# Kernel tuning notes

Hardware: AMD Instinct MI355X
Metric: run time of the kernel (lower is better)

The kernel has to match this reference:

```python
import jax, jax.numpy as jnp
import numpy as np
import math

B, S, D, H = 2, 2048, 1024, 16
DK = D // H


def setup_inputs() -> dict:
    key = jax.random.key(0)
    ks = jax.random.split(key, 11)
    f = jnp.float32
    return {
        "query": jax.random.normal(ks[0], (B, S, D), f),
        "key": jax.random.normal(ks[1], (B, S, D), f),
        "value": jax.random.normal(ks[2], (B, S, D), f),
        "wq": jax.random.normal(ks[3], (D, D), f) * 0.02,
        "bq": jnp.zeros((D,), f),
        "wk": jax.random.normal(ks[4], (D, D), f) * 0.02,
        "bk": jnp.zeros((D,), f),
        "wv": jax.random.normal(ks[5], (D, D), f) * 0.02,
        "bv": jnp.zeros((D,), f),
        "wo": jax.random.normal(ks[6], (D, D), f) * 0.02,
        "bo": jnp.zeros((D,), f),
    }


def reference(query, key, value, wq, bq, wk, bk, wv, bv, wo, bo):
    # Linear projections (torch Linear: y = x @ W.T + b)
    q = query @ wq.T + bq
    k = key @ wk.T + bk
    v = value @ wv.T + bv
    # [B,S,D] -> [B,H,S,DK]
    q = q.reshape(B, S, H, DK).transpose(0, 2, 1, 3)
    k = k.reshape(B, S, H, DK).transpose(0, 2, 1, 3)
    v = v.reshape(B, S, H, DK).transpose(0, 2, 1, 3)
    scores = jnp.einsum("bhqd,bhkd->bhqk", q, k) / math.sqrt(DK)
    causal = jnp.triu(jnp.ones((S, S), dtype=bool), k=1)  # strict upper triangle masked
    scores = jnp.where(causal, -jnp.inf, scores)
    attn = jax.nn.softmax(scores, axis=-1)  # dropout is identity in eval (p=0)
    x = jnp.einsum("bhqk,bhkd->bhqd", attn, v)
    x = x.transpose(0, 2, 1, 3).reshape(B, S, D)
    return x @ wo.T + bo
```

## Files before the change

kernel.cpp:

```cpp
#include <hip/hip_runtime.h>
#include <math.h>

#define BB 2
#define SS 2048
#define DD 1024
#define HH 16
#define DKK 64
#define MM (BB * SS)
#define KK DD
#define VSTR 2176

typedef __attribute__((ext_vector_type(8))) short short8;
typedef __attribute__((ext_vector_type(4))) float floatx4;

__device__ inline unsigned short f2bf(float x) {
    unsigned int u = __float_as_uint(x);
    u += 0x7fffu + ((u >> 16) & 1u);
    return (unsigned short)(u >> 16);
}

__device__ inline unsigned int pkbf(float a, float b) {
    return (__float_as_uint(b) & 0xffff0000u) | (__float_as_uint(a) >> 16);
}

__device__ inline unsigned int pkbf_rne(float a, float b) {
    return (unsigned int)f2bf(a) | ((unsigned int)f2bf(b) << 16);
}

__device__ inline unsigned int cvtpk(float a, float b) {
    unsigned int r;
    asm("v_cvt_pk_bf16_f32 %0, %1, %2" : "=v"(r) : "v"(a), "v"(b));
    return r;
}

__device__ inline void cast4f(const float* __restrict__ in, unsigned short* __restrict__ out, int i) {
    const float4 v = *(const float4*)(in + i);
    unsigned long long pk = (unsigned long long)f2bf(v.x)
                          | ((unsigned long long)f2bf(v.y) << 16)
                          | ((unsigned long long)f2bf(v.z) << 32)
                          | ((unsigned long long)f2bf(v.w) << 48);
    *(unsigned long long*)(out + i) = pk;
}

__global__ __launch_bounds__(256) void cast_all(const float* __restrict__ q, const float* __restrict__ k,
                                                const float* __restrict__ v,
                                                const float* __restrict__ wq, const float* __restrict__ wk,
                                                const float* __restrict__ wv, const float* __restrict__ wo,
                                                unsigned short* __restrict__ oq, unsigned short* __restrict__ ok,
                                                unsigned short* __restrict__ ov,
                                                unsigned short* __restrict__ owq, unsigned short* __restrict__ owk,
                                                unsigned short* __restrict__ owv, unsigned short* __restrict__ owo) {
    const int blk = blockIdx.x;
    const float* in;
    unsigned short* out;
    int idx;
    if (blk < 12288) {
        const int w = blk >> 12;
        idx = blk & 4095;
        in  = (w == 0) ? q : (w == 1) ? k : v;
        out = (w == 0) ? oq : (w == 1) ? ok : ov;
    } else {
        const int w = (blk - 12288) >> 10;
        idx = (blk - 12288) & 1023;
        in  = (w == 0) ? wq : (w == 1) ? wk : (w == 2) ? wv : wo;
        out = (w == 0) ? owq : (w == 1) ? owk : (w == 2) ? owv : owo;
    }
    cast4f(in, out, (idx * 256 + threadIdx.x) * 4);
}

#define GLDS(gp, lp) __builtin_amdgcn_global_load_lds( \
    (const __attribute__((address_space(1))) void*)(gp), \
    (__attribute__((address_space(3))) void*)(lp), 16, 0, 0)

#define SCHED0() __builtin_amdgcn_sched_barrier(0)
#define BAR()    __builtin_amdgcn_s_barrier()
#define WAITL0() asm volatile("s_waitcnt lgkmcnt(0)" ::: "memory")
#define WAITV(n) asm volatile("s_waitcnt vmcnt(" #n ")" ::: "memory")

template<int BN, int SWAP>
__device__ __forceinline__ void gemm_body2(const unsigned short* __restrict__ A,
                                           const unsigned short* __restrict__ W,
                                           int m0, int n0,
                                           unsigned short* __restrict__ As,
                                           unsigned short* __restrict__ Bs,
                                           floatx4 (&acc)[4][BN / 32]) {
    constexpr int NJ = BN / 32;
    const int t    = threadIdx.x;
    const int lane = t & 63;
    const int wave = t >> 6;
    const int col  = lane & 15;
    const int quad = lane >> 4;
    const int wm   = (wave >> 1) * 64;
    const int wn   = (wave & 1) * (BN / 2);

    const int r  = t >> 3;
    const int cs = t & 7;

    const int sA0 = (quad ^ (col & 7)) * 8;
    const int sA1 = ((quad + 4) ^ (col & 7)) * 8;

    auto stage = [&](int kt, int pb) {
        const int k0 = kt * 64;
        #pragma unroll
        for (int g = 0; g < 4; ++g) {
            const int row = g * 32 + r;
            const int ksw = (cs ^ (row & 7)) * 8;
            GLDS(A + (size_t)(m0 + row) * KK + k0 + ksw,
                 &As[pb * (128 * 64) + row * 64 + cs * 8]);
        }
        #pragma unroll
        for (int g = 0; g < BN / 32; ++g) {
            const int row = g * 32 + r;
            const int ksw = (cs ^ (row & 7)) * 8;
            GLDS(W + (size_t)(n0 + row) * KK + k0 + ksw,
                 &Bs[pb * (BN * 64) + row * 64 + cs * 8]);
        }
    };

    const int NK = KK / 64;

    auto tile_step = [&](int kt, int p) {
        if (kt + 1 < NK) stage(kt + 1, p ^ 1);

        const unsigned short* Ab = &As[p * (128 * 64)];
        const unsigned short* Bb = &Bs[p * (BN * 64)];
        short8 a0[4], a1[4], b0[NJ], b1[NJ];
        #pragma unroll
        for (int i = 0; i < 4; ++i) {
            const unsigned short* ar = Ab + (wm + i * 16 + col) * 64;
            a0[i] = *(const short8*)(ar + sA0);
            a1[i] = *(const short8*)(ar + sA1);
        }
        #pragma unroll
        for (int j = 0; j < NJ; ++j) {
            const unsigned short* br = Bb + (wn + j * 16 + col) * 64;
            b0[j] = *(const short8*)(br + sA0);
            b1[j] = *(const short8*)(br + sA1);
        }

        __builtin_amdgcn_s_setprio(1);
        #pragma unroll
        for (int i = 0; i < 4; ++i)
            #pragma unroll
            for (int j = 0; j < NJ; ++j) {
                if constexpr (SWAP)
                    acc[i][j] = __builtin_amdgcn_mfma_f32_16x16x32_bf16(b0[j], a0[i], acc[i][j], 0, 0, 0);
                else
                    acc[i][j] = __builtin_amdgcn_mfma_f32_16x16x32_bf16(a0[i], b0[j], acc[i][j], 0, 0, 0);
            }
        #pragma unroll
        for (int i = 0; i < 4; ++i)
            #pragma unroll
            for (int j = 0; j < NJ; ++j) {
                if constexpr (SWAP)
                    acc[i][j] = __builtin_amdgcn_mfma_f32_16x16x32_bf16(b1[j], a1[i], acc[i][j], 0, 0, 0);
                else
                    acc[i][j] = __builtin_amdgcn_mfma_f32_16x16x32_bf16(a1[i], b1[j], acc[i][j], 0, 0, 0);
            }
        __builtin_amdgcn_s_setprio(0);

        WAITL0(); SCHED0();
        if (kt + 1 < NK) { WAITV(0); }
        SCHED0(); BAR(); SCHED0();
    };

    stage(0, 0);
    WAITV(0); SCHED0(); BAR(); SCHED0();

    #pragma unroll 1
    for (int kt = 0; kt < NK; kt += 2) {
        tile_step(kt, 0);
        tile_step(kt + 1, 1);
    }
}

__global__ __launch_bounds__(256, 2) void gemm_qkv(const unsigned short* __restrict__ qB,
                                                   const unsigned short* __restrict__ kB,
                                                   const unsigned short* __restrict__ vB,
                                                   const unsigned short* __restrict__ wqB,
                                                   const unsigned short* __restrict__ wkB,
                                                   const unsigned short* __restrict__ wvB,
                                                   const float* __restrict__ bq,
                                                   const float* __restrict__ bk,
                                                   const float* __restrict__ bv,
                                                   unsigned short* __restrict__ Qh,
                                                   unsigned short* __restrict__ Kh,
                                                   unsigned short* __restrict__ Vt) {
    __shared__ __align__(16) unsigned short As[2 * 128 * 64];
    __shared__ __align__(16) unsigned short Bs[2 * 128 * 64];

    const int bid   = blockIdx.x;
    const int wgid  = (bid & 7) * 96 + (bid >> 3);
    const int which = wgid >> 8;
    const int tile  = wgid & 255;
    const int m0    = (tile >> 3) * 128;
    const int n0    = (tile & 7) * 128;

    const unsigned short* A = (which == 0) ? qB : (which == 1) ? kB : vB;
    const unsigned short* W = (which == 0) ? wqB : (which == 1) ? wkB : wvB;
    const float* bias       = (which == 0) ? bq : (which == 1) ? bk : bv;

    const int t    = threadIdx.x;
    const int lane = t & 63;
    const int wave = t >> 6;
    const int col  = lane & 15;
    const int quad = lane >> 4;
    const int wm   = (wave >> 1) * 64;
    const int wn   = (wave & 1) * 64;

    floatx4 acc[4][4] = {};

    if (which != 2) {
        gemm_body2<128, 1>(A, W, m0, n0, As, Bs, acc);
        unsigned short* O = (which == 0) ? Qh : Kh;
        #pragma unroll
        for (int i = 0; i < 4; ++i) {
            const int mb  = m0 + wm + i * 16 + col;
            const int bdx = mb >> 11, s = mb & 2047;
            #pragma unroll
            for (int j = 0; j < 4; ++j) {
                const int n  = n0 + wn + j * 16 + quad * 4;
                const float4 b4 = *(const float4*)(bias + n);
                const int h = n >> 6, dk = n & 63;
                uint2 w;
                w.x = pkbf_rne(acc[i][j][0] + b4.x, acc[i][j][1] + b4.y);
                w.y = pkbf_rne(acc[i][j][2] + b4.z, acc[i][j][3] + b4.w);
                *(uint2*)(O + (((size_t)(bdx * HH + h)) * SS + s) * DKK + dk) = w;
            }
        }
    } else {
        gemm_body2<128, 0>(A, W, m0, n0, As, Bs, acc);
        #pragma unroll
        for (int i = 0; i < 4; ++i) {
            #pragma unroll
            for (int j = 0; j < 4; ++j) {
                const int n  = n0 + wn + j * 16 + col;
                const float bv0 = bias[n];
                const int h = n >> 6, dk = n & 63;
                const int mb  = m0 + wm + i * 16 + quad * 4;
                const int bdx = mb >> 11, s = mb & 2047;
                unsigned short* vp = Vt + (((size_t)(bdx * HH + h)) * DKK + dk) * VSTR + s;
                uint2 w;
                w.x = pkbf_rne(acc[i][j][0] + bv0, acc[i][j][1] + bv0);
                w.y = pkbf_rne(acc[i][j][2] + bv0, acc[i][j][3] + bv0);
                *(uint2*)vp = w;
            }
        }
    }
}

__global__ __launch_bounds__(256, 2) void gemm_out(const unsigned short* __restrict__ A,
                                                   const unsigned short* __restrict__ W,
                                                   const float* __restrict__ bias,
                                                   float* __restrict__ C) {
    __shared__ __align__(16) unsigned short As[2 * 128 * 64];
    __shared__ __align__(16) unsigned short Bs[2 * 64 * 64];

    const int bid  = blockIdx.x;
    const int wgid = (bid & 7) * 64 + (bid >> 3);
    const int m0   = (wgid >> 4) * 128;
    const int n0   = (wgid & 15) * 64;

    floatx4 acc[4][2] = {};
    gemm_body2<64, 0>(A, W, m0, n0, As, Bs, acc);

    const int t    = threadIdx.x;
    const int lane = t & 63;
    const int wave = t >> 6;
    const int col  = lane & 15;
    const int quad = lane >> 4;
    const int wm   = (wave >> 1) * 64;
    const int wn   = (wave & 1) * 32;

    #pragma unroll
    for (int i = 0; i < 4; ++i) {
        #pragma unroll
        for (int j = 0; j < 2; ++j) {
            const int n = n0 + wn + j * 16 + col;
            const float bv0 = bias[n];
            #pragma unroll
            for (int rr = 0; rr < 4; ++rr) {
                const int m = m0 + wm + i * 16 + quad * 4 + rr;
                C[(size_t)m * DD + n] = acc[i][j][rr] + bv0;
            }
        }
    }
}

#define C1 0.18033688011112042f
#define C2 11.541560327111707f
#define MFMA __builtin_amdgcn_mfma_f32_16x16x32_bf16

__global__ __launch_bounds__(512, 4) void attn_mfma(const unsigned short* __restrict__ Qh,
                                                    const unsigned short* __restrict__ Kh,
                                                    const unsigned short* __restrict__ Vt,
                                                    unsigned short* __restrict__ X) {
    __shared__ __align__(16) unsigned short Ks[2][64 * 64];
    __shared__ __align__(16) unsigned short Vs[2][64 * 64];
    __shared__ __align__(16) unsigned short Plds[8][16 * 40];

    const int t    = threadIdx.x;
    const int lane = t & 63;
    const int wave = t >> 6;
    const int col  = lane & 15;
    const int quad = lane >> 4;

    const int lin = blockIdx.x;
    const int bh  = (lin & 7) + 8 * ((lin >> 3) & 3);
    const int pr  = lin >> 5;
    const int b   = bh / HH, h = bh % HH;

    const int cX  = (wave < 4) ? (31 - pr) : pr;
    const int q0  = cX * 64 + (wave & 3) * 16;
    const int nst = 32 - pr;

    const unsigned short* Kb = Kh + (size_t)bh * SS * DKK;
    const unsigned short* Vb = Vt + (size_t)bh * DKK * VSTR;

    const int r0  = t >> 3;
    const int sg0 = ((t & 7) ^ (r0 & 7)) * 8;

    unsigned short* Pw = &Plds[wave][0];

    const unsigned short* Qb = Qh + ((size_t)bh * SS + q0) * DKK;
    const short8 qa0 = *(const short8*)(Qb + (size_t)col * DKK + quad * 8);
    const short8 qa1 = *(const short8*)(Qb + (size_t)col * DKK + 32 + quad * 8);

    floatx4 o0 = {0.f, 0.f, 0.f, 0.f}, o1 = o0, o2 = o0, o3 = o0;
    floatx4 olp = {0.f, 0.f, 0.f, 0.f};

    const short8 vone = { (short)0x3F80, (short)0x3F80, (short)0x3F80, (short)0x3F80,
                          (short)0x3F80, (short)0x3F80, (short)0x3F80, (short)0x3F80 };

    const int ksA = ((quad)      ^ (col & 7)) * 8;
    const int ksB = ((quad | 4)  ^ (col & 7)) * 8;

    auto half_body = [&](const unsigned short* Kp, const unsigned short* Vp, int kb) {
        #pragma unroll
        for (int hh = 0; hh < 2; ++hh) {
            const int j0 = kb * 64 + hh * 32;
            if (j0 < q0 + 16) {
                const short8 k0 = *(const short8*)(Kp + (hh * 32 + col) * 64 + ksA);
                const short8 k1 = *(const short8*)(Kp + (hh * 32 + col) * 64 + ksB);
                const short8 k2 = *(const short8*)(Kp + (hh * 32 + col + 16) * 64 + ksA);
                const short8 k3 = *(const short8*)(Kp + (hh * 32 + col + 16) * 64 + ksB);

                floatx4 t0 = {0.f, 0.f, 0.f, 0.f}, t1 = t0;
                __builtin_amdgcn_s_setprio(1);
                t0 = MFMA(k0, qa0, t0, 0, 0, 0);
                t0 = MFMA(k1, qa1, t0, 0, 0, 0);
                t1 = MFMA(k2, qa0, t1, 0, 0, 0);
                t1 = MFMA(k3, qa1, t1, 0, 0, 0);
                __builtin_amdgcn_s_setprio(0);

                float p[8];
                if (j0 + 31 > q0) {
                    const int lim = q0 + col - j0;
                    #pragma unroll
                    for (int rr = 0; rr < 4; ++rr) {
                        p[rr]     = (quad * 4 + rr      <= lim) ? __builtin_exp2f(fmaf(t0[rr], C1, -C2)) : 0.f;
                        p[4 + rr] = (16 + quad * 4 + rr <= lim) ? __builtin_exp2f(fmaf(t1[rr], C1, -C2)) : 0.f;
                    }
                } else {
                    #pragma unroll
                    for (int rr = 0; rr < 4; ++rr) {
                        p[rr]     = __builtin_exp2f(fmaf(t0[rr], C1, -C2));
                        p[4 + rr] = __builtin_exp2f(fmaf(t1[rr], C1, -C2));
                    }
                }

                uint2 w0 = { cvtpk(p[0], p[1]), cvtpk(p[2], p[3]) };
                uint2 w1 = { cvtpk(p[4], p[5]), cvtpk(p[6], p[7]) };
                *(uint2*)(Pw + col * 40 + quad * 4)      = w0;
                *(uint2*)(Pw + col * 40 + 16 + quad * 4) = w1;

                const short8 pb = *(const short8*)(Pw + col * 40 + quad * 8);
                const int vs = hh ? ksB : ksA;
                const short8 v0 = *(const short8*)(Vp + (col)      * 64 + vs);
                const short8 v1 = *(const short8*)(Vp + (col + 16) * 64 + vs);
                const short8 v2 = *(const short8*)(Vp + (col + 32) * 64 + vs);
                const short8 v3 = *(const short8*)(Vp + (col + 48) * 64 + vs);
                __builtin_amdgcn_s_setprio(1);
                o0  = MFMA(v0, pb, o0, 0, 0, 0);
                o1  = MFMA(v1, pb, o1, 0, 0, 0);
                o2  = MFMA(v2, pb, o2, 0, 0, 0);
                o3  = MFMA(v3, pb, o3, 0, 0, 0);
                olp = MFMA(vone, pb, olp, 0, 0, 0);
                __builtin_amdgcn_s_setprio(0);
            }
        }
    };

    auto step = [&](int kb, int cur) {
        __syncthreads();
        if (kb + 1 < nst) {
            const int jn = (kb + 1) * 64;
            const int nx = cur ^ 1;
            GLDS(Kb + (size_t)(jn + r0) * DKK + sg0,  &Ks[nx][t * 8]);
            GLDS(Vb + (size_t)r0 * VSTR + jn + sg0,   &Vs[nx][t * 8]);
        }
        half_body(&Ks[cur][0], &Vs[cur][0], kb);
    };

    GLDS(Kb + (size_t)r0 * DKK + sg0,  &Ks[0][t * 8]);
    GLDS(Vb + (size_t)r0 * VSTR + sg0, &Vs[0][t * 8]);

    #pragma unroll 1
    for (int kb = 0; kb < nst; kb += 2) {
        step(kb, 0);
        if (kb + 1 < nst) step(kb + 1, 1);
    }

    const float li = 1.f / olp[0];

    unsigned short* Xp = X + ((size_t)(b * SS + q0 + col)) * DD + h * DKK + quad * 4;
    {
        uint2 w;
        w.x = cvtpk(o0[0] * li, o0[1] * li);
        w.y = cvtpk(o0[2] * li, o0[3] * li);
        *(uint2*)(Xp + 0) = w;
        w.x = cvtpk(o1[0] * li, o1[1] * li);
        w.y = cvtpk(o1[2] * li, o1[3] * li);
        *(uint2*)(Xp + 16) = w;
        w.x = cvtpk(o2[0] * li, o2[1] * li);
        w.y = cvtpk(o2[2] * li, o2[3] * li);
        *(uint2*)(Xp + 32) = w;
        w.x = cvtpk(o3[0] * li, o3[1] * li);
        w.y = cvtpk(o3[2] * li, o3[3] * li);
        *(uint2*)(Xp + 48) = w;
    }
}

extern "C" void kernel_launch(void* const* d_in, const int* in_sizes, int n_in,
                              void* d_out, int out_size, void* d_ws, size_t ws_size,
                              hipStream_t stream) {
    const float* query = (const float*)d_in[0];
    const float* key   = (const float*)d_in[1];
    const float* value = (const float*)d_in[2];
    const float* wq    = (const float*)d_in[3];
    const float* bq    = (const float*)d_in[4];
    const float* wk    = (const float*)d_in[5];
    const float* bk    = (const float*)d_in[6];
    const float* wv    = (const float*)d_in[7];
    const float* bv    = (const float*)d_in[8];
    const float* wo    = (const float*)d_in[9];
    const float* bo    = (const float*)d_in[10];

    char* ws = (char*)d_ws;
    const size_t MB = 1024 * 1024;
    unsigned short* qB  = (unsigned short*)(ws);
    unsigned short* kB  = (unsigned short*)(ws + 8 * MB);
    unsigned short* vB  = (unsigned short*)(ws + 16 * MB);
    unsigned short* wqB = (unsigned short*)(ws + 24 * MB);
    unsigned short* wkB = (unsigned short*)(ws + 26 * MB);
    unsigned short* wvB = (unsigned short*)(ws + 28 * MB);
    unsigned short* woB = (unsigned short*)(ws + 30 * MB);
    unsigned short* Qh  = (unsigned short*)(ws + 32 * MB);
    unsigned short* Kh  = (unsigned short*)(ws + 40 * MB);
    unsigned short* Vt  = (unsigned short*)(ws + 48 * MB);
    unsigned short* Xb  = qB;

    cast_all<<<16384, 256, 0, stream>>>(query, key, value, wq, wk, wv, wo,
                                        qB, kB, vB, wqB, wkB, wvB, woB);

    gemm_qkv<<<768, 256, 0, stream>>>(qB, kB, vB, wqB, wkB, wvB, bq, bk, bv, Qh, Kh, Vt);

    attn_mfma<<<512, 512, 0, stream>>>(Qh, Kh, Vt, Xb);

    gemm_out<<<512, 256, 0, stream>>>(Xb, woB, bo, (float*)d_out);
}
```

Baseline: 208.6 us.

## Shrink QKV GEMM M-tile and stage two KV blocks per attention sync

Result: no change. 205.0 us, median of 2 (-1.7%).

```diff
diff --git a/kernel.cpp b/kernel.cpp
--- a/kernel.cpp
+++ b/kernel.cpp
@@ -17,10 +17,6 @@
     unsigned int u = __float_as_uint(x);
     u += 0x7fffu + ((u >> 16) & 1u);
     return (unsigned short)(u >> 16);
-}
-
-__device__ inline unsigned int pkbf(float a, float b) {
-    return (__float_as_uint(b) & 0xffff0000u) | (__float_as_uint(a) >> 16);
 }
 
 __device__ inline unsigned int pkbf_rne(float a, float b) {
@@ -77,20 +73,21 @@
 #define WAITL0() asm volatile("s_waitcnt lgkmcnt(0)" ::: "memory")
 #define WAITV(n) asm volatile("s_waitcnt vmcnt(" #n ")" ::: "memory")
 
-template<int BN, int SWAP>
+template<int BM, int BN, int SWAP>
 __device__ __forceinline__ void gemm_body2(const unsigned short* __restrict__ A,
                                            const unsigned short* __restrict__ W,
                                            int m0, int n0,
                                            unsigned short* __restrict__ As,
                                            unsigned short* __restrict__ Bs,
-                                           floatx4 (&acc)[4][BN / 32]) {
+                                           floatx4 (&acc)[BM / 32][BN / 32]) {
+    constexpr int NI = BM / 32;
     constexpr int NJ = BN / 32;
     const int t    = threadIdx.x;
     const int lane = t & 63;
     const int wave = t >> 6;
     const int col  = lane & 15;
     const int quad = lane >> 4;
-    const int wm   = (wave >> 1) * 64;
+    const int wm   = (wave >> 1) * (BM / 2);
     const int wn   = (wave & 1) * (BN / 2);
 
     const int r  = t >> 3;
@@ -102,11 +99,11 @@
     auto stage = [&](int kt, int pb) {
         const int k0 = kt * 64;
         #pragma unroll
-        for (int g = 0; g < 4; ++g) {
+        for (int g = 0; g < BM / 32; ++g) {
             const int row = g * 32 + r;
             const int ksw = (cs ^ (row & 7)) * 8;
             GLDS(A + (size_t)(m0 + row) * KK + k0 + ksw,
-                 &As[pb * (128 * 64) + row * 64 + cs * 8]);
+                 &As[pb * (BM * 64) + row * 64 + cs * 8]);
         }
         #pragma unroll
         for (int g = 0; g < BN / 32; ++g) {
@@ -122,11 +119,11 @@
     auto tile_step = [&](int kt, int p) {
         if (kt + 1 < NK) stage(kt + 1, p ^ 1);
 
-        const unsigned short* Ab = &As[p * (128 * 64)];
+        const unsigned short* Ab = &As[p * (BM * 64)];
         const unsigned short* Bb = &Bs[p * (BN * 64)];
-        short8 a0[4], a1[4], b0[NJ], b1[NJ];
-        #pragma unroll
-        for (int i = 0; i < 4; ++i) {
+        short8 a0[NI], a1[NI], b0[NJ], b1[NJ];
+        #pragma unroll
+        for (int i = 0; i < NI; ++i) {
             const unsigned short* ar = Ab + (wm + i * 16 + col) * 64;
             a0[i] = *(const short8*)(ar + sA0);
             a1[i] = *(const short8*)(ar + sA1);
@@ -140,7 +137,7 @@
 
         __builtin_amdgcn_s_setprio(1);
         #pragma unroll
-        for (int i = 0; i < 4; ++i)
+        for (int i = 0; i < NI; ++i)
             #pragma unroll
             for (int j = 0; j < NJ; ++j) {
                 if constexpr (SWAP)
@@ -149,7 +146,7 @@
                     acc[i][j] = __builtin_amdgcn_mfma_f32_16x16x32_bf16(a0[i], b0[j], acc[i][j], 0, 0, 0);
             }
         #pragma unroll
-        for (int i = 0; i < 4; ++i)
+        for (int i = 0; i < NI; ++i)
             #pragma unroll
             for (int j = 0; j < NJ; ++j) {
                 if constexpr (SWAP)
@@ -174,7 +171,7 @@
     }
 }
 
-__global__ __launch_bounds__(256, 2) void gemm_qkv(const unsigned short* __restrict__ qB,
+__global__ __launch_bounds__(256, 3) void gemm_qkv(const unsigned short* __restrict__ qB,
                                                    const unsigned short* __restrict__ kB,
                                                    const unsigned short* __restrict__ vB,
                                                    const unsigned short* __restrict__ wqB,
@@ -186,14 +183,14 @@
                                                    unsigned short* __restrict__ Qh,
                                                    unsigned short* __restrict__ Kh,
                                                    unsigned short* __restrict__ Vt) {
-    __shared__ __align__(16) unsigned short As[2 * 128 * 64];
+    __shared__ __align__(16) unsigned short As[2 * 64 * 64];
     __shared__ __align__(16) unsigned short Bs[2 * 128 * 64];
 
     const int bid   = blockIdx.x;
-    const int wgid  = (bid & 7) * 96 + (bid >> 3);
-    const int which = wgid >> 8;
-    const int tile  = wgid & 255;
-    const int m0    = (tile >> 3) * 128;
+    const int wgid  = (bid & 7) * 192 + (bid >> 3);
+    const int which = wgid >> 9;
+    const int tile  = wgid & 511;
+    const int m0    = (tile >> 3) * 64;
     const int n0    = (tile & 7) * 128;
 
     const unsigned short* A = (which == 0) ? qB : (which == 1) ? kB : vB;
@@ -205,16 +202,16 @@
     const int wave = t >> 6;
     const int col  = lane & 15;
     const int quad = lane >> 4;
-    const int wm   = (wave >> 1) * 64;
+    const int wm   = (wave >> 1) * 32;
     const int wn   = (wave & 1) * 64;
 
-    floatx4 acc[4][4] = {};
+    floatx4 acc[2][4] = {};
 
     if (which != 2) {
-        gemm_body2<128, 1>(A, W, m0, n0, As, Bs, acc);
+        gemm_body2<64, 128, 1>(A, W, m0, n0, As, Bs, acc);
         unsigned short* O = (which == 0) ? Qh : Kh;
         #pragma unroll
-        for (int i = 0; i < 4; ++i) {
+        for (int i = 0; i < 2; ++i) {
             const int mb  = m0 + wm + i * 16 + col;
             const int bdx = mb >> 11, s = mb & 2047;
             #pragma unroll
@@ -229,9 +226,9 @@
             }
         }
     } else {
-        gemm_body2<128, 0>(A, W, m0, n0, As, Bs, acc);
-        #pragma unroll
-        for (int i = 0; i < 4; ++i) {
+        gemm_body2<64, 128, 0>(A, W, m0, n0, As, Bs, acc);
+        #pragma unroll
+        for (int i = 0; i < 2; ++i) {
             #pragma unroll
             for (int j = 0; j < 4; ++j) {
                 const int n  = n0 + wn + j * 16 + col;
@@ -262,7 +259,7 @@
     const int n0   = (wgid & 15) * 64;
 
     floatx4 acc[4][2] = {};
-    gemm_body2<64, 0>(A, W, m0, n0, As, Bs, acc);
+    gemm_body2<128, 64, 0>(A, W, m0, n0, As, Bs, acc);
 
     const int t    = threadIdx.x;
     const int lane = t & 63;
@@ -295,8 +292,8 @@
                                                     const unsigned short* __restrict__ Kh,
                                                     const unsigned short* __restrict__ Vt,
                                                     unsigned short* __restrict__ X) {
-    __shared__ __align__(16) unsigned short Ks[2][64 * 64];
-    __shared__ __align__(16) unsigned short Vs[2][64 * 64];
+    __shared__ __align__(16) unsigned short Ks[2][2 * 64 * 64];
+    __shared__ __align__(16) unsigned short Vs[2][2 * 64 * 64];
     __shared__ __align__(16) unsigned short Plds[8][16 * 40];
 
     const int t    = threadIdx.x;
@@ -334,6 +331,12 @@
 
     const int ksA = ((quad)      ^ (col & 7)) * 8;
     const int ksB = ((quad | 4)  ^ (col & 7)) * 8;
+
+    auto stage64 = [&](int kb, int buf, int sub) {
+        const int jn = kb * 64;
+        GLDS(Kb + (size_t)(jn + r0) * DKK + sg0, &Ks[buf][sub * 4096 + t * 8]);
+        GLDS(Vb + (size_t)r0 * VSTR + jn + sg0,  &Vs[buf][sub * 4096 + t * 8]);
+    };
 
     auto half_body = [&](const unsigned short* Kp, const unsigned short* Vp, int kb) {
         #pragma unroll
@@ -391,24 +394,24 @@
         }
     };
 
-    auto step = [&](int kb, int cur) {
+    const int nsteps = (nst + 1) >> 1;
+
+    auto step = [&](int s, int cur) {
         __syncthreads();
-        if (kb + 1 < nst) {
-            const int jn = (kb + 1) * 64;
-            const int nx = cur ^ 1;
-            GLDS(Kb + (size_t)(jn + r0) * DKK + sg0,  &Ks[nx][t * 8]);
-            GLDS(Vb + (size_t)r0 * VSTR + jn + sg0,   &Vs[nx][t * 8]);
-        }
-        half_body(&Ks[cur][0], &Vs[cur][0], kb);
+        const int kbn = 2 * s + 2;
+        if (kbn < nst)     stage64(kbn,     cur ^ 1, 0);
+        if (kbn + 1 < nst) stage64(kbn + 1, cur ^ 1, 1);
+        half_body(&Ks[cur][0],    &Vs[cur][0],    2 * s);
+        half_body(&Ks[cur][4096], &Vs[cur][4096], 2 * s + 1);
     };
 
-    GLDS(Kb + (size_t)r0 * DKK + sg0,  &Ks[0][t * 8]);
-    GLDS(Vb + (size_t)r0 * VSTR + sg0, &Vs[0][t * 8]);
+    stage64(0, 0, 0);
+    stage64(1, 0, 1);
 
     #pragma unroll 1
-    for (int kb = 0; kb < nst; kb += 2) {
-        step(kb, 0);
-        if (kb + 1 < nst) step(kb + 1, 1);
+    for (int s = 0; s < nsteps; s += 2) {
+        step(s, 0);
+        if (s + 1 < nsteps) step(s + 1, 1);
     }
 
     const float li = 1.f / olp[0];
@@ -463,7 +466,7 @@
     cast_all<<<16384, 256, 0, stream>>>(query, key, value, wq, wk, wv, wo,
                                         qB, kB, vB, wqB, wkB, wvB, woB);
 
-    gemm_qkv<<<768, 256, 0, stream>>>(qB, kB, vB, wqB, wkB, wvB, bq, bk, bv, Qh, Kh, Vt);
+    gemm_qkv<<<1536, 256, 0, stream>>>(qB, kB, vB, wqB, wkB, wvB, bq, bk, bv, Qh, Kh, Vt);
 
     attn_mfma<<<512, 512, 0, stream>>>(Qh, Kh, Vt, Xb);
 
```
